# Kernel tuning notes

Hardware: AMD Instinct MI355X
Metric: run time of the kernel (lower is better)

The kernel has to match this reference:

```python
import jax, jax.numpy as jnp
import numpy as np

NUM_CLASSES = 80
RESO = 416
ANCHORS = np.array([[116.0, 90.0], [156.0, 198.0], [373.0, 326.0]], dtype=np.float32)  # (nA, 2)


def setup_inputs() -> dict:
    key = jax.random.key(0)
    bs, gs = 512, 13
    nA = ANCHORS.shape[0]
    num_attrs = 5 + NUM_CLASSES
    x = jax.random.normal(key, (bs, nA * num_attrs, gs, gs), dtype=jnp.float32)
    return {"x": x}


def reference(x):
    # YOLO detection-head decode (inference path of YOLOLayer.forward)
    bs, _, gs, _ = x.shape
    stride = RESO // gs
    nA = ANCHORS.shape[0]
    num_attrs = 5 + NUM_CLASSES
    scaled_anchors = jnp.asarray(ANCHORS) / jnp.float32(stride)  # (nA, 2)

    # (bs, nA, num_attrs, gs, gs) -> (bs, nA, gs, gs, num_attrs)
    xr = x.reshape(bs, nA, num_attrs, gs, gs).transpose(0, 1, 3, 4, 2)

    pred_tx = jax.nn.sigmoid(xr[..., 0])
    pred_ty = jax.nn.sigmoid(xr[..., 1])
    pred_tw = xr[..., 2]
    pred_th = xr[..., 3]
    pred_conf = jax.nn.sigmoid(xr[..., 4])
    pred_cls = jax.nn.softmax(xr[..., 5:], axis=-1)

    grid = jnp.arange(gs, dtype=jnp.float32)
    grid_x = grid[None, None, None, :]  # varies along last grid axis (i)
    grid_y = grid[None, None, :, None]  # varies along row axis (j)
    anchor_w = scaled_anchors[:, 0][None, :, None, None]
    anchor_h = scaled_anchors[:, 1][None, :, None, None]

    s = jnp.float32(stride)
    bx = (pred_tx + grid_x) * s
    by = (pred_ty + grid_y) * s
    bw = jnp.exp(pred_tw) * anchor_w * s
    bh = jnp.exp(pred_th) * anchor_h * s

    pred = jnp.concatenate(
        [bx[..., None], by[..., None], bw[..., None], bh[..., None],
         pred_conf[..., None], pred_cls],
        axis=-1,
    )  # (bs, nA, gs, gs, num_attrs)
    return pred.reshape(bs, -1, num_attrs)
```

## Files before the change

kernel.cpp:

```cpp
#include <hip/hip_runtime.h>
#include <math.h>

namespace {

constexpr int kBS      = 512;
constexpr int kNA      = 3;
constexpr int kGS      = 13;
constexpr int kAttrs   = 85;
constexpr int kSpatial = kGS * kGS;
constexpr int kCells   = kBS * kNA * kSpatial;
constexpr float kStrideF = 32.0f;

constexpr int kBlockThreads = 128;
constexpr int kCellsPerBlock = kBlockThreads;
constexpr int kSmemFloats = kCellsPerBlock * kAttrs;
constexpr int kSmemFloat4 = kSmemFloats / 4;

__device__ __forceinline__ float fsigmoid(float x) {
    return 1.0f / (1.0f + __expf(-x));
}

__global__ __launch_bounds__(kBlockThreads) void yolo_head_kernel(const float* __restrict__ x,
                                                                  float* __restrict__ out) {
    __shared__ float smem[kSmemFloats];

    const int tid  = threadIdx.x;
    const int cell = blockIdx.x * kCellsPerBlock + tid;

    const int s  = cell % kSpatial;
    const int ba = cell / kSpatial;
    const int a  = ba % kNA;

    const float* __restrict__ xp = x + (size_t)ba * kAttrs * kSpatial + s;

    float v[kAttrs];
#pragma unroll
    for (int c = 0; c < kAttrs; ++c) {
        v[c] = xp[(size_t)c * kSpatial];
    }

    const float jf  = (float)(s % kGS);
    const float if_ = (float)(s / kGS);

    const float aw = (a == 0) ? 116.0f : (a == 1) ? 156.0f : 373.0f;
    const float ah = (a == 0) ?  90.0f : (a == 1) ? 198.0f : 326.0f;

    float* __restrict__ sp = smem + tid * kAttrs;

    sp[0] = (fsigmoid(v[0]) + jf) * kStrideF;
    sp[1] = (fsigmoid(v[1]) + if_) * kStrideF;
    sp[2] = __expf(v[2]) * aw;
    sp[3] = __expf(v[3]) * ah;
    sp[4] = fsigmoid(v[4]);

    float m = v[5];
#pragma unroll
    for (int c = 6; c < kAttrs; ++c) m = fmaxf(m, v[c]);
    float sum = 0.0f;
#pragma unroll
    for (int c = 5; c < kAttrs; ++c) {
        const float e = __expf(v[c] - m);
        v[c] = e;
        sum += e;
    }
    const float inv = 1.0f / sum;
#pragma unroll
    for (int c = 5; c < kAttrs; ++c) sp[c] = v[c] * inv;

    __syncthreads();

    float4* __restrict__ out4 = (float4*)(out + (size_t)blockIdx.x * kSmemFloats);
    const float4* __restrict__ s4 = (const float4*)smem;
#pragma unroll 4
    for (int t = tid; t < kSmemFloat4; t += kBlockThreads) {
        out4[t] = s4[t];
    }
}

}

extern "C" void kernel_launch(void* const* d_in, const int* in_sizes, int n_in,
                              void* d_out, int out_size, void* d_ws, size_t ws_size,
                              hipStream_t stream) {
    const float* x = (const float*)d_in[0];
    float* out = (float*)d_out;
    const int blocks = kCells / kCellsPerBlock;
    yolo_head_kernel<<<blocks, kBlockThreads, 0, stream>>>(x, out);
}
```

Measured before the change: 37.48 us.

## Stage output through double-buffered 32-cell shared memory chunks

Shrinks the shared-memory staging buffer from a whole block's worth of cells to two 32-cell chunks. Results stay in registers, and each wavefront-sized group writes its chunk in turn while the block streams the previous chunk to global memory. The aim is less LDS per block, so more blocks can be resident. The cost is extra barriers, serialized staging across groups, and longer register lifetimes for the 85 values, which may raise register pressure.

```diff
diff --git a/kernel.cpp b/kernel.cpp
--- a/kernel.cpp
+++ b/kernel.cpp
@@ -11,10 +11,12 @@
 constexpr int kCells   = kBS * kNA * kSpatial;
 constexpr float kStrideF = 32.0f;
 
-constexpr int kBlockThreads = 128;
-constexpr int kCellsPerBlock = kBlockThreads;
-constexpr int kSmemFloats = kCellsPerBlock * kAttrs;
-constexpr int kSmemFloat4 = kSmemFloats / 4;
+constexpr int kBlockThreads  = 128;
+constexpr int kChunkCells    = 32;
+constexpr int kNumChunks     = kBlockThreads / kChunkCells;
+constexpr int kChunkFloats   = kChunkCells * kAttrs;
+constexpr int kChunkFloat4   = kChunkFloats / 4;
+constexpr int kBlockFloats   = kBlockThreads * kAttrs;
 
 __device__ __forceinline__ float fsigmoid(float x) {
     return 1.0f / (1.0f + __expf(-x));
@@ -22,10 +24,10 @@
 
 __global__ __launch_bounds__(kBlockThreads) void yolo_head_kernel(const float* __restrict__ x,
                                                                   float* __restrict__ out) {
-    __shared__ float smem[kSmemFloats];
+    __shared__ float smem[2][kChunkFloats];
 
     const int tid  = threadIdx.x;
-    const int cell = blockIdx.x * kCellsPerBlock + tid;
+    const int cell = blockIdx.x * kBlockThreads + tid;
 
     const int s  = cell % kSpatial;
     const int ba = cell / kSpatial;
@@ -45,13 +47,11 @@
     const float aw = (a == 0) ? 116.0f : (a == 1) ? 156.0f : 373.0f;
     const float ah = (a == 0) ?  90.0f : (a == 1) ? 198.0f : 326.0f;
 
-    float* __restrict__ sp = smem + tid * kAttrs;
-
-    sp[0] = (fsigmoid(v[0]) + jf) * kStrideF;
-    sp[1] = (fsigmoid(v[1]) + if_) * kStrideF;
-    sp[2] = __expf(v[2]) * aw;
-    sp[3] = __expf(v[3]) * ah;
-    sp[4] = fsigmoid(v[4]);
+    v[0] = (fsigmoid(v[0]) + jf) * kStrideF;
+    v[1] = (fsigmoid(v[1]) + if_) * kStrideF;
+    v[2] = __expf(v[2]) * aw;
+    v[3] = __expf(v[3]) * ah;
+    v[4] = fsigmoid(v[4]);
 
     float m = v[5];
 #pragma unroll
@@ -65,15 +65,33 @@
     }
     const float inv = 1.0f / sum;
 #pragma unroll
-    for (int c = 5; c < kAttrs; ++c) sp[c] = v[c] * inv;
+    for (int c = 5; c < kAttrs; ++c) v[c] *= inv;
 
+    const int group = tid >> 5;
+    const int lane  = tid & 31;
+
+    auto stage = [&](int k) {
+        if (group == k) {
+            float* __restrict__ sp = &smem[k & 1][lane * kAttrs];
+#pragma unroll
+            for (int c = 0; c < kAttrs; ++c) sp[c] = v[c];
+        }
+    };
+
+    stage(0);
     __syncthreads();
 
-    float4* __restrict__ out4 = (float4*)(out + (size_t)blockIdx.x * kSmemFloats);
-    const float4* __restrict__ s4 = (const float4*)smem;
-#pragma unroll 4
-    for (int t = tid; t < kSmemFloat4; t += kBlockThreads) {
-        out4[t] = s4[t];
+    for (int k = 0; k < kNumChunks; ++k) {
+        if (k < kNumChunks - 1) stage(k + 1);
+
+        const float4* __restrict__ s4 = (const float4*)smem[k & 1];
+        float4* __restrict__ out4 =
+            (float4*)(out + (size_t)blockIdx.x * kBlockFloats + (size_t)k * kChunkFloats);
+#pragma unroll
+        for (int t = tid; t < kChunkFloat4; t += kBlockThreads) {
+            out4[t] = s4[t];
+        }
+        __syncthreads();
     }
 }
 
@@ -84,6 +102,6 @@
                               hipStream_t stream) {
     const float* x = (const float*)d_in[0];
     float* out = (float*)d_out;
-    const int blocks = kCells / kCellsPerBlock;
+    const int blocks = kCells / kBlockThreads;
     yolo_head_kernel<<<blocks, kBlockThreads, 0, stream>>>(x, out);
 }
```

After: 38.09 us. About the same (+1.6%).

## Split each cell's attributes across four threads with shuffle softmax reduction

Applied to the files above, without the earlier changes.

Each detection cell is now handled by four cooperating threads, each loading a strided quarter of the 85 attributes. The softmax max and sum are combined with warp shuffles, and the box and confidence terms are spread across the four lanes. This cuts per-thread register pressure from 85 values to 22 and raises the number of threads in flight, at the cost of extra shuffles and more scattered per-lane global loads. Block size grows to 256 threads covering 64 cells, so shared memory per block shrinks.

```diff
diff --git a/kernel.cpp b/kernel.cpp
--- a/kernel.cpp
+++ b/kernel.cpp
@@ -3,18 +3,19 @@
 
 namespace {
 
-constexpr int kBS      = 512;
 constexpr int kNA      = 3;
 constexpr int kGS      = 13;
 constexpr int kAttrs   = 85;
 constexpr int kSpatial = kGS * kGS;
-constexpr int kCells   = kBS * kNA * kSpatial;
+constexpr int kCells   = 512 * kNA * kSpatial;
 constexpr float kStrideF = 32.0f;
 
-constexpr int kBlockThreads = 128;
-constexpr int kCellsPerBlock = kBlockThreads;
-constexpr int kSmemFloats = kCellsPerBlock * kAttrs;
-constexpr int kSmemFloat4 = kSmemFloats / 4;
+constexpr int kBlockThreads  = 256;
+constexpr int kThreadsPerCell = 4;
+constexpr int kCellsPerBlock = kBlockThreads / kThreadsPerCell;
+constexpr int kSmemFloats    = kCellsPerBlock * kAttrs;
+constexpr int kSmemFloat4    = kSmemFloats / 4;
+constexpr int kMaxAttrsPerThread = 22;
 
 __device__ __forceinline__ float fsigmoid(float x) {
     return 1.0f / (1.0f + __expf(-x));
@@ -25,7 +26,9 @@
     __shared__ float smem[kSmemFloats];
 
     const int tid  = threadIdx.x;
-    const int cell = blockIdx.x * kCellsPerBlock + tid;
+    const int q    = tid & 3;
+    const int cl   = tid >> 2;
+    const int cell = blockIdx.x * kCellsPerBlock + cl;
 
     const int s  = cell % kSpatial;
     const int ba = cell / kSpatial;
@@ -33,45 +36,62 @@
 
     const float* __restrict__ xp = x + (size_t)ba * kAttrs * kSpatial + s;
 
-    float v[kAttrs];
+    float v[kMaxAttrsPerThread];
 #pragma unroll
-    for (int c = 0; c < kAttrs; ++c) {
-        v[c] = xp[(size_t)c * kSpatial];
+    for (int i = 0; i < kMaxAttrsPerThread; ++i) {
+        const int c = q + 4 * i;
+        if (c < kAttrs) v[i] = xp[(size_t)c * kSpatial];
     }
 
-    const float jf  = (float)(s % kGS);
-    const float if_ = (float)(s / kGS);
+    float m = -INFINITY;
+#pragma unroll
+    for (int i = 0; i < kMaxAttrsPerThread; ++i) {
+        const int c = q + 4 * i;
+        if (c >= 5 && c < kAttrs) m = fmaxf(m, v[i]);
+    }
+    m = fmaxf(m, __shfl_xor(m, 1, 64));
+    m = fmaxf(m, __shfl_xor(m, 2, 64));
 
-    const float aw = (a == 0) ? 116.0f : (a == 1) ? 156.0f : 373.0f;
-    const float ah = (a == 0) ?  90.0f : (a == 1) ? 198.0f : 326.0f;
-
-    float* __restrict__ sp = smem + tid * kAttrs;
-
-    sp[0] = (fsigmoid(v[0]) + jf) * kStrideF;
-    sp[1] = (fsigmoid(v[1]) + if_) * kStrideF;
-    sp[2] = __expf(v[2]) * aw;
-    sp[3] = __expf(v[3]) * ah;
-    sp[4] = fsigmoid(v[4]);
-
-    float m = v[5];
-#pragma unroll
-    for (int c = 6; c < kAttrs; ++c) m = fmaxf(m, v[c]);
     float sum = 0.0f;
 #pragma unroll
-    for (int c = 5; c < kAttrs; ++c) {
-        const float e = __expf(v[c] - m);
-        v[c] = e;
-        sum += e;
+    for (int i = 0; i < kMaxAttrsPerThread; ++i) {
+        const int c = q + 4 * i;
+        if (c >= 5 && c < kAttrs) {
+            v[i] = __expf(v[i] - m);
+            sum += v[i];
+        }
     }
+    sum += __shfl_xor(sum, 1, 64);
+    sum += __shfl_xor(sum, 2, 64);
     const float inv = 1.0f / sum;
+
+    float* __restrict__ sp = smem + cl * kAttrs;
+
+    if (q == 0) {
+        const float jf = (float)(s % kGS);
+        sp[0] = (fsigmoid(v[0]) + jf) * kStrideF;
+        sp[4] = fsigmoid(v[1]);
+    } else if (q == 1) {
+        const float if_ = (float)(s / kGS);
+        sp[1] = (fsigmoid(v[0]) + if_) * kStrideF;
+    } else if (q == 2) {
+        const float aw = (a == 0) ? 116.0f : (a == 1) ? 156.0f : 373.0f;
+        sp[2] = __expf(v[0]) * aw;
+    } else {
+        const float ah = (a == 0) ? 90.0f : (a == 1) ? 198.0f : 326.0f;
+        sp[3] = __expf(v[0]) * ah;
+    }
 #pragma unroll
-    for (int c = 5; c < kAttrs; ++c) sp[c] = v[c] * inv;
+    for (int i = 0; i < kMaxAttrsPerThread; ++i) {
+        const int c = q + 4 * i;
+        if (c >= 5 && c < kAttrs) sp[c] = v[i] * inv;
+    }
 
     __syncthreads();
 
+    const float4* __restrict__ s4 = (const float4*)smem;
     float4* __restrict__ out4 = (float4*)(out + (size_t)blockIdx.x * kSmemFloats);
-    const float4* __restrict__ s4 = (const float4*)smem;
-#pragma unroll 4
+#pragma unroll 2
     for (int t = tid; t < kSmemFloat4; t += kBlockThreads) {
         out4[t] = s4[t];
     }
```

Measured after the change: 39.83 us. 1.06x slower.

## Stream class exps to LDS, defer softmax normalization to copy-out, shrink blocks

Applied to the files above, without the earlier changes.

Drops the 85-float per-thread register array. Each thread now writes box terms and unnormalized class exponentials straight into shared memory and stores only its reciprocal sum. The vectorized copy-out applies the per-cell scale on the fly and uses nontemporal stores, with blocks halved to 64 threads. The max-subtraction pass is removed, which avoids the extra reduction but risks exp overflow for large logits.

```diff
diff --git a/kernel.cpp b/kernel.cpp
--- a/kernel.cpp
+++ b/kernel.cpp
@@ -3,77 +3,80 @@
 
 namespace {
 
-constexpr int kBS      = 512;
 constexpr int kNA      = 3;
 constexpr int kGS      = 13;
 constexpr int kAttrs   = 85;
 constexpr int kSpatial = kGS * kGS;
-constexpr int kCells   = kBS * kNA * kSpatial;
+constexpr int kCells   = 512 * kNA * kSpatial;
 constexpr float kStrideF = 32.0f;
 
-constexpr int kBlockThreads = 128;
-constexpr int kCellsPerBlock = kBlockThreads;
-constexpr int kSmemFloats = kCellsPerBlock * kAttrs;
-constexpr int kSmemFloat4 = kSmemFloats / 4;
+constexpr int kT          = 64;
+constexpr int kSmemFloats = kT * kAttrs;
+constexpr int kSmemF4     = kSmemFloats / 4;
+
+using f32x4 = __attribute__((ext_vector_type(4))) float;
 
 __device__ __forceinline__ float fsigmoid(float x) {
     return 1.0f / (1.0f + __expf(-x));
 }
 
-__global__ __launch_bounds__(kBlockThreads) void yolo_head_kernel(const float* __restrict__ x,
-                                                                  float* __restrict__ out) {
+__global__ __launch_bounds__(kT) void yolo_head_kernel(const float* __restrict__ x,
+                                                       float* __restrict__ out) {
     __shared__ float smem[kSmemFloats];
+    __shared__ float inv_s[kT];
 
     const int tid  = threadIdx.x;
-    const int cell = blockIdx.x * kCellsPerBlock + tid;
+    const int cell = blockIdx.x * kT + tid;
 
     const int s  = cell % kSpatial;
     const int ba = cell / kSpatial;
     const int a  = ba % kNA;
 
     const float* __restrict__ xp = x + (size_t)ba * kAttrs * kSpatial + s;
+    float* __restrict__ sp = smem + tid * kAttrs;
 
-    float v[kAttrs];
-#pragma unroll
-    for (int c = 0; c < kAttrs; ++c) {
-        v[c] = xp[(size_t)c * kSpatial];
+    {
+        const float t0 = xp[0];
+        const float t1 = xp[kSpatial];
+        const float t2 = xp[2 * kSpatial];
+        const float t3 = xp[3 * kSpatial];
+        const float t4 = xp[4 * kSpatial];
+        const float aw = (a == 0) ? 116.0f : (a == 1) ? 156.0f : 373.0f;
+        const float ah = (a == 0) ?  90.0f : (a == 1) ? 198.0f : 326.0f;
+        sp[0] = (fsigmoid(t0) + (float)(s % kGS)) * kStrideF;
+        sp[1] = (fsigmoid(t1) + (float)(s / kGS)) * kStrideF;
+        sp[2] = __expf(t2) * aw;
+        sp[3] = __expf(t3) * ah;
+        sp[4] = fsigmoid(t4);
     }
 
-    const float jf  = (float)(s % kGS);
-    const float if_ = (float)(s / kGS);
-
-    const float aw = (a == 0) ? 116.0f : (a == 1) ? 156.0f : 373.0f;
-    const float ah = (a == 0) ?  90.0f : (a == 1) ? 198.0f : 326.0f;
-
-    float* __restrict__ sp = smem + tid * kAttrs;
-
-    sp[0] = (fsigmoid(v[0]) + jf) * kStrideF;
-    sp[1] = (fsigmoid(v[1]) + if_) * kStrideF;
-    sp[2] = __expf(v[2]) * aw;
-    sp[3] = __expf(v[3]) * ah;
-    sp[4] = fsigmoid(v[4]);
-
-    float m = v[5];
-#pragma unroll
-    for (int c = 6; c < kAttrs; ++c) m = fmaxf(m, v[c]);
     float sum = 0.0f;
 #pragma unroll
     for (int c = 5; c < kAttrs; ++c) {
-        const float e = __expf(v[c] - m);
-        v[c] = e;
+        const float e = __expf(xp[(size_t)c * kSpatial]);
+        sp[c] = e;
         sum += e;
     }
-    const float inv = 1.0f / sum;
-#pragma unroll
-    for (int c = 5; c < kAttrs; ++c) sp[c] = v[c] * inv;
+    inv_s[tid] = 1.0f / sum;
 
     __syncthreads();
 
-    float4* __restrict__ out4 = (float4*)(out + (size_t)blockIdx.x * kSmemFloats);
-    const float4* __restrict__ s4 = (const float4*)smem;
-#pragma unroll 4
-    for (int t = tid; t < kSmemFloat4; t += kBlockThreads) {
-        out4[t] = s4[t];
+    const f32x4* __restrict__ s4 = (const f32x4*)smem;
+    f32x4* __restrict__ o4 = (f32x4*)(out + (size_t)blockIdx.x * kSmemFloats);
+
+    int k0 = 4 * tid;
+    int cl = (k0 >= 170) ? 2 : (k0 >= 85 ? 1 : 0);
+    int c2 = k0 - 85 * cl;
+    for (int t = tid; t < kSmemF4; t += kT) {
+        f32x4 d = s4[t];
+        const float inv = inv_s[cl];
+        d.x *= (c2 >= 5)               ? inv : 1.0f;
+        d.y *= (c2 >= 4 && c2 <= 83)   ? inv : 1.0f;
+        d.z *= (c2 >= 3 && c2 <= 82)   ? inv : 1.0f;
+        d.w *= (c2 >= 2 && c2 <= 81)   ? inv : 1.0f;
+        __builtin_nontemporal_store(d, &o4[t]);
+        cl += 3; c2 += 1;
+        if (c2 >= 85) { c2 -= 85; ++cl; }
     }
 }
 
@@ -84,6 +87,6 @@
                               hipStream_t stream) {
     const float* x = (const float*)d_in[0];
     float* out = (float*)d_out;
-    const int blocks = kCells / kCellsPerBlock;
-    yolo_head_kernel<<<blocks, kBlockThreads, 0, stream>>>(x, out);
+    const int blocks = kCells / kT;
+    yolo_head_kernel<<<blocks, kT, 0, stream>>>(x, out);
 }
```

Result: slower. 39.60 us (+5.6%).
